# Optimization experiments

Hardware: AMD Instinct MI355X
Metric: run time of the kernel (lower is better)

## Reference

```python
import jax, jax.numpy as jnp
import numpy as np

NUM_HEADS = 12
HEAD_DIM = 64  # d_out // num_heads = 768 // 12


def setup_inputs() -> dict:
    key = jax.random.key(0)
    ks = jax.random.split(key, 6)
    b, s, d = 2, 2048, 768
    x = jax.random.normal(ks[0], (b, s, d), dtype=jnp.float32)
    sc = 1.0 / np.sqrt(d)
    Wq = jax.random.normal(ks[1], (d, d), dtype=jnp.float32) * sc
    Wk = jax.random.normal(ks[2], (d, d), dtype=jnp.float32) * sc
    Wv = jax.random.normal(ks[3], (d, d), dtype=jnp.float32) * sc
    Wo = jax.random.normal(ks[4], (d, d), dtype=jnp.float32) * sc
    bo = jnp.zeros((d,), dtype=jnp.float32)
    return {"x": x, "Wq": Wq, "Wk": Wk, "Wv": Wv, "Wo": Wo, "bo": bo}


def reference(x, Wq, Wk, Wv, Wo, bo):
    # Prefill from a fresh sliding-window KV cache: cache == new K/V,
    # standard causal (triu) mask. dropout=0 (eval).
    b, s, d = x.shape
    H, Dh = NUM_HEADS, HEAD_DIM

    def proj(W):  # torch Linear: x @ W^T, then split heads -> [b, H, s, Dh]
        return (x @ W.T).reshape(b, s, H, Dh).transpose(0, 2, 1, 3)

    q, k, v = proj(Wq), proj(Wk), proj(Wv)

    scores = jnp.einsum('bhqd,bhkd->bhqk', q, k)          # [b,H,s,s]
    causal = jnp.triu(jnp.ones((s, s), dtype=bool), k=1)  # future positions
    scores = jnp.where(causal[None, None], -jnp.inf, scores)
    attn = jax.nn.softmax(scores / np.sqrt(Dh), axis=-1)

    ctx = jnp.einsum('bhqk,bhkd->bhqd', attn, v)          # [b,H,s,Dh]
    ctx = ctx.transpose(0, 2, 1, 3).reshape(b, s, d)      # [b,s,d_out]
    return ctx @ Wo.T + bo
```

## Files before the change

### kernel.cpp

```cpp
#include <hip/hip_runtime.h>
#include <stdint.h>

typedef __attribute__((ext_vector_type(4))) float f32x4;
typedef __attribute__((ext_vector_type(8))) short s16x8;

#if __has_builtin(__builtin_amdgcn_exp2f)
#define EXP2(x) __builtin_amdgcn_exp2f(x)
#else
#define EXP2(x) exp2f(x)
#endif

#define GL2LDS(g, s)                                                        \
  __builtin_amdgcn_global_load_lds(                                         \
      (const __attribute__((address_space(1))) void*)(g),                   \
      (__attribute__((address_space(3))) void*)(s), 16, 0, 0)

__device__ __forceinline__ unsigned short tobf(float x) {
  uint32_t u = __builtin_bit_cast(uint32_t, x);
  u += 0x7fffu + ((u >> 16) & 1u);
  return (unsigned short)(u >> 16);
}

__device__ __forceinline__ uint32_t pk2(float lo, float hi) {
  return (uint32_t)tobf(lo) | ((uint32_t)tobf(hi) << 16);
}

__device__ __forceinline__ uint32_t pktrunc(float lo, float hi) {
  return __builtin_amdgcn_perm(__builtin_bit_cast(uint32_t, hi),
                               __builtin_bit_cast(uint32_t, lo), 0x07060302u);
}

__global__ __launch_bounds__(256) void cvt_all(
    const float* __restrict__ x,  const float* __restrict__ wq,
    const float* __restrict__ wk, const float* __restrict__ wv,
    const float* __restrict__ wo, unsigned short* __restrict__ outb) {
  int i = blockIdx.x * 256 + threadIdx.x;
  if (i >= 1376256) return;
  const float* in;
  int j;
  if (i < 786432) { in = x; j = i; }
  else {
    int k = i - 786432;
    int sel = k / 147456;
    j = k - sel * 147456;
    in = (sel == 0) ? wq : (sel == 1) ? wk : (sel == 2) ? wv : wo;
  }
  float4 v = reinterpret_cast<const float4*>(in)[j];
  uint2 o; o.x = pk2(v.x, v.y); o.y = pk2(v.z, v.w);
  reinterpret_cast<uint2*>(outb)[i] = o;
}

__global__ __launch_bounds__(128) void qkv_gemm(
    const unsigned short* __restrict__ xb,
    const unsigned short* __restrict__ wq,
    const unsigned short* __restrict__ wk,
    const unsigned short* __restrict__ wv,
    unsigned short* __restrict__ q_ws,
    unsigned short* __restrict__ k_ws,
    unsigned short* __restrict__ vt_ws) {
  __shared__ unsigned short As[2][2048];
  __shared__ unsigned short Bs[2][4096];
  const int t = threadIdx.x;
  const int l = t & 63, w = t >> 6;
  const int lr = l & 15, lg = l >> 4;

  const int id = (int)blockIdx.x;
  const int xcd = id & 7;
  const int g = id >> 3;
  const int nt = g % 18;
  const int tileM = ((g / 18) * 8 + xcd) * 64;
  const int wsel = nt / 6;
  const unsigned short* W = (wsel == 0) ? wq : ((wsel == 1) ? wk : wv);
  const int tileN = (nt % 6) * 128;

  const int srow = w * 16 + (l >> 2);
  const int scol = ((l & 3) ^ ((l >> 2) & 3)) * 8;

#define QSTAGE(buf, k0_)                                                       \
  do {                                                                         \
    GL2LDS(&xb[(tileM + srow) * 768 + (k0_) + scol],       &As[buf][w * 512]); \
    GL2LDS(&xb[(tileM + 32 + srow) * 768 + (k0_) + scol],  &As[buf][1024 + w * 512]); \
    _Pragma("unroll")                                                          \
    for (int i_ = 0; i_ < 4; ++i_)                                             \
      GL2LDS(&W[(tileN + i_ * 32 + srow) * 768 + (k0_) + scol],                \
             &Bs[buf][i_ * 1024 + w * 512]);                                   \
  } while (0)

  const int chf = ((lg ^ (lr & 3)) << 3);

  f32x4 acc[4][4];
  const f32x4 z4 = {0.f, 0.f, 0.f, 0.f};
#pragma unroll
  for (int i = 0; i < 4; ++i)
#pragma unroll
    for (int j = 0; j < 4; ++j) acc[i][j] = z4;

  QSTAGE(0, 0);
  __syncthreads();
  int c = 0;
  for (int it = 0; it < 24; ++it) {
    if (it < 23) QSTAGE(c ^ 1, (it + 1) * 32);
    s16x8 a[4], b[4];
#pragma unroll
    for (int mi = 0; mi < 4; ++mi)
      a[mi] = *(const s16x8*)&As[c][(mi * 16 + lr) * 32 + chf];
#pragma unroll
    for (int ni = 0; ni < 4; ++ni)
      b[ni] = *(const s16x8*)&Bs[c][(w * 64 + ni * 16 + lr) * 32 + chf];
    __builtin_amdgcn_s_setprio(1);
#pragma unroll
    for (int mi = 0; mi < 4; ++mi)
#pragma unroll
      for (int ni = 0; ni < 4; ++ni)
        acc[mi][ni] = __builtin_amdgcn_mfma_f32_16x16x32_bf16(a[mi], b[ni], acc[mi][ni], 0, 0, 0);
    __builtin_amdgcn_s_setprio(0);
    if (it < 23) {
      __syncthreads();
      c ^= 1;
    }
  }
#undef QSTAGE

#pragma unroll
  for (int mi = 0; mi < 4; ++mi)
#pragma unroll
    for (int ni = 0; ni < 4; ++ni) {
      int m0 = tileM + mi * 16 + lg * 4;
      int n = tileN + w * 64 + ni * 16 + lr;
      int bb = m0 >> 11, sq0 = m0 & 2047;
      int h = n >> 6, dh = n & 63;
      if (wsel == 0) {
#pragma unroll
        for (int r = 0; r < 4; ++r)
          q_ws[((bb * 12 + h) * 2048 + sq0 + r) * 64 + dh] =
              tobf(acc[mi][ni][r] * 0.18033688011112042f);
      } else if (wsel == 1) {
#pragma unroll
        for (int r = 0; r < 4; ++r)
          k_ws[((bb * 12 + h) * 2048 + sq0 + r) * 64 + dh] = tobf(acc[mi][ni][r]);
      } else {
        uint2 o;
        o.x = pk2(acc[mi][ni][0], acc[mi][ni][1]);
        o.y = pk2(acc[mi][ni][2], acc[mi][ni][3]);
        *(uint2*)&vt_ws[((bb * 12 + h) * 64 + dh) * 2048 + sq0] = o;
      }
    }
}

__global__ __launch_bounds__(128) void attn_kernel(
    const unsigned short* __restrict__ q_ws,
    const unsigned short* __restrict__ k_ws,
    const unsigned short* __restrict__ vt_ws,
    unsigned short* __restrict__ ctx) {
  __shared__ unsigned short Ks[2][4096];
  __shared__ unsigned short Vs[2][4096];

  const int t = threadIdx.x;
  const int l = t & 63, w = t >> 6;
  const int lr = l & 15, lg = l >> 4;

  const int id = (int)blockIdx.x;
  const int xcd = id & 7;
  const int g = id >> 3;
  const int qt = 63 - g / 3;
  const int bh = (g % 3) * 8 + xcd;

  const int rb = w * 8 + (l >> 3);
  const int gcol = ((l & 7) ^ (l >> 3)) * 8;
  const int krow = 8 * ((rb >> 2) & 3) + (rb & 3);
  const unsigned short* kgp  = &k_ws[(bh * 2048 + krow) * 64 + gcol];
  const unsigned short* vbase = &vt_ws[(bh * 64 + rb) * 2048 + gcol];

#define STAGE(buf, kt_)                                                \
  do {                                                                 \
    GL2LDS(kgp + (kt_) * 4096,           &Ks[buf][w * 512]);           \
    GL2LDS(kgp + (kt_) * 4096 + 2048,    &Ks[buf][1024 + w * 512]);    \
    GL2LDS(kgp + (kt_) * 4096 + 256,     &Ks[buf][2048 + w * 512]);    \
    GL2LDS(kgp + (kt_) * 4096 + 2304,    &Ks[buf][3072 + w * 512]);    \
    GL2LDS(vbase + (kt_) * 64,           &Vs[buf][w * 512]);           \
    GL2LDS(vbase + (kt_) * 64 + 32768,   &Vs[buf][1024 + w * 512]);    \
    GL2LDS(vbase + (kt_) * 64 + 65536,   &Vs[buf][2048 + w * 512]);    \
    GL2LDS(vbase + (kt_) * 64 + 98304,   &Vs[buf][3072 + w * 512]);    \
  } while (0)

  const int cks0 = (lg * 8) ^ ((lr & 7) << 3);
  const int cks1 = (32 + lg * 8) ^ ((lr & 7) << 3);

  const int bb = bh / 12, hh = bh % 12;
  const f32x4 z4 = {0.f, 0.f, 0.f, 0.f};

  const int ktmax = qt >> 1;
  const int qg = qt * 32 + w * 16 + lr;

  s16x8 qa[2];
#pragma unroll
  for (int kk = 0; kk < 2; ++kk)
    qa[kk] = *(const s16x8*)&q_ws[(bh * 2048 + qg) * 64 + kk * 32 + lg * 8];

  f32x4 o[4];
#pragma unroll
  for (int di = 0; di < 4; ++di) o[di] = z4;
  float lrun = 0.f;
  f32x4 s[4];

  STAGE(0, 0);
  __syncthreads();

  __builtin_amdgcn_s_setprio(1);
#pragma unroll
  for (int ni = 0; ni < 4; ++ni) {
    s16x8 kb0 = *(const s16x8*)&Ks[0][ni * 1024 + lr * 64 + cks0];
    s16x8 kb1 = *(const s16x8*)&Ks[0][ni * 1024 + lr * 64 + cks1];
    s[ni] = __builtin_amdgcn_mfma_f32_16x16x32_bf16(kb0, qa[0], z4, 0, 0, 0);
    s[ni] = __builtin_amdgcn_mfma_f32_16x16x32_bf16(kb1, qa[1], s[ni], 0, 0, 0);
  }
  __builtin_amdgcn_s_setprio(0);
  if (ktmax >= 1) STAGE(1, 1);

  int c = 0;
  for (int kt = 0; kt <= ktmax; ++kt) {
    if (kt == ktmax) {
#pragma unroll
      for (int ni = 0; ni < 4; ++ni)
#pragma unroll
        for (int r = 0; r < 4; ++r) {
          int kg_ = kt * 64 + ((ni & 1) << 5) + (lg << 3) + ((ni >> 1) << 2) + r;
          if (kg_ > qg) s[ni][r] = -1e30f;
        }
    }

#pragma unroll
    for (int ni = 0; ni < 4; ++ni)
#pragma unroll
      for (int r = 0; r < 4; ++r) s[ni][r] = EXP2(s[ni][r]);
    {
      float t0 = (s[0][0] + s[0][1]) + (s[0][2] + s[0][3]);
      float t1 = (s[1][0] + s[1][1]) + (s[1][2] + s[1][3]);
      float t2 = (s[2][0] + s[2][1]) + (s[2][2] + s[2][3]);
      float t3 = (s[3][0] + s[3][1]) + (s[3][2] + s[3][3]);
      lrun += (t0 + t1) + (t2 + t3);
    }

    s16x8 pa[2];
#pragma unroll
    for (int kk = 0; kk < 2; ++kk) {
      uint4 u;
      u.x = pktrunc(s[kk][0],     s[kk][1]);
      u.y = pktrunc(s[kk][2],     s[kk][3]);
      u.z = pktrunc(s[kk + 2][0], s[kk + 2][1]);
      u.w = pktrunc(s[kk + 2][2], s[kk + 2][3]);
      pa[kk] = __builtin_bit_cast(s16x8, u);
    }

    const bool have_next = (kt < ktmax);
    __builtin_amdgcn_s_setprio(1);
    if (have_next) {
      __syncthreads();
#pragma unroll
      for (int ni = 0; ni < 4; ++ni) {
        s16x8 kb0 = *(const s16x8*)&Ks[c ^ 1][ni * 1024 + lr * 64 + cks0];
        s16x8 kb1 = *(const s16x8*)&Ks[c ^ 1][ni * 1024 + lr * 64 + cks1];
        s[ni] = __builtin_amdgcn_mfma_f32_16x16x32_bf16(kb0, qa[0], z4, 0, 0, 0);
        s[ni] = __builtin_amdgcn_mfma_f32_16x16x32_bf16(kb1, qa[1], s[ni], 0, 0, 0);
      }
    }
#pragma unroll
    for (int di = 0; di < 4; ++di) {
      s16x8 vb0 = *(const s16x8*)&Vs[c][di * 1024 + lr * 64 + cks0];
      s16x8 vb1 = *(const s16x8*)&Vs[c][di * 1024 + lr * 64 + cks1];
      o[di] = __builtin_amdgcn_mfma_f32_16x16x32_bf16(vb0, pa[0], o[di], 0, 0, 0);
      o[di] = __builtin_amdgcn_mfma_f32_16x16x32_bf16(vb1, pa[1], o[di], 0, 0, 0);
    }
    __builtin_amdgcn_s_setprio(0);

    if (kt + 2 <= ktmax) {
      __syncthreads();
      STAGE(c, kt + 2);
    }
    c ^= 1;
  }

  float lt = lrun + __shfl_xor(lrun, 16);
  lt += __shfl_xor(lt, 32);
  const float rl = 1.0f / lt;
#pragma unroll
  for (int di = 0; di < 4; ++di) {
    uint2 ov;
    ov.x = pk2(o[di][0] * rl, o[di][1] * rl);
    ov.y = pk2(o[di][2] * rl, o[di][3] * rl);
    *(uint2*)&ctx[(bb * 2048 + qg) * 768 + hh * 64 + di * 16 + lg * 4] = ov;
  }
#undef STAGE
}

__global__ __launch_bounds__(64) void out_gemm(
    const unsigned short* __restrict__ ctxb,
    const unsigned short* __restrict__ wo,
    const float* __restrict__ bo,
    float* __restrict__ out) {
  __shared__ unsigned short As[2][2048];
  __shared__ unsigned short Bs[2][2048];
  const int l = threadIdx.x;
  const int lr = l & 15, lg = l >> 4;

  const int id = (int)blockIdx.x;
  const int xcd = id & 7;
  const int g = id >> 3;
  const int tileN = (g % 12) * 64;
  const int tileM = ((g / 12) * 8 + xcd) * 64;

  const int srow = l >> 2;
  const int scol = ((l & 3) ^ (srow & 3)) * 8;

#define OSTAGE(buf, k0_)                                                       \
  do {                                                                         \
    _Pragma("unroll")                                                          \
    for (int i_ = 0; i_ < 4; ++i_) {                                           \
      GL2LDS(&ctxb[(tileM + i_ * 16 + srow) * 768 + (k0_) + scol],             \
             &As[buf][i_ * 512]);                                              \
      GL2LDS(&wo  [(tileN + i_ * 16 + srow) * 768 + (k0_) + scol],             \
             &Bs[buf][i_ * 512]);                                              \
    }                                                                          \
  } while (0)

  const int chf = ((lg ^ (lr & 3)) << 3);

  f32x4 acc[4][4];
  const f32x4 z4 = {0.f, 0.f, 0.f, 0.f};
#pragma unroll
  for (int i = 0; i < 4; ++i)
#pragma unroll
    for (int j = 0; j < 4; ++j) acc[i][j] = z4;

  OSTAGE(0, 0);
  __syncthreads();
  int c = 0;
  for (int it = 0; it < 24; ++it) {
    if (it < 23) OSTAGE(c ^ 1, (it + 1) * 32);
    s16x8 a[4], b[4];
#pragma unroll
    for (int mi = 0; mi < 4; ++mi)
      a[mi] = *(const s16x8*)&As[c][(mi * 16 + lr) * 32 + chf];
#pragma unroll
    for (int ni = 0; ni < 4; ++ni)
      b[ni] = *(const s16x8*)&Bs[c][(ni * 16 + lr) * 32 + chf];
    __builtin_amdgcn_s_setprio(1);
#pragma unroll
    for (int mi = 0; mi < 4; ++mi)
#pragma unroll
      for (int ni = 0; ni < 4; ++ni)
        acc[mi][ni] = __builtin_amdgcn_mfma_f32_16x16x32_bf16(a[mi], b[ni], acc[mi][ni], 0, 0, 0);
    __builtin_amdgcn_s_setprio(0);
    if (it < 23) {
      __syncthreads();
      c ^= 1;
    }
  }
#undef OSTAGE

#pragma unroll
  for (int mi = 0; mi < 4; ++mi)
#pragma unroll
    for (int ni = 0; ni < 4; ++ni)
#pragma unroll
      for (int r = 0; r < 4; ++r) {
        int m = tileM + mi * 16 + lg * 4 + r;
        int n = tileN + ni * 16 + lr;
        out[m * 768 + n] = acc[mi][ni][r] + bo[n];
      }
}

extern "C" void kernel_launch(void* const* d_in, const int* in_sizes, int n_in,
                              void* d_out, int out_size, void* d_ws, size_t ws_size,
                              hipStream_t stream) {
  const float* x  = (const float*)d_in[0];
  const float* Wq = (const float*)d_in[1];
  const float* Wk = (const float*)d_in[2];
  const float* Wv = (const float*)d_in[3];
  const float* Wo = (const float*)d_in[4];
  const float* bo = (const float*)d_in[5];
  float* out = (float*)d_out;

  char* ws = (char*)d_ws;
  unsigned short* xb    = (unsigned short*)(ws);
  unsigned short* wqb   = (unsigned short*)(ws + 6291456);
  unsigned short* wkb   = (unsigned short*)(ws + 7471104);
  unsigned short* wvb   = (unsigned short*)(ws + 8650752);
  unsigned short* wob   = (unsigned short*)(ws + 9830400);
  unsigned short* q_ws  = (unsigned short*)(ws + 11010048);
  unsigned short* k_ws  = (unsigned short*)(ws + 17301504);
  unsigned short* vt_ws = (unsigned short*)(ws + 23592960);
  unsigned short* ctx   = (unsigned short*)(ws + 29884416);

  cvt_all<<<5376, 256, 0, stream>>>(x, Wq, Wk, Wv, Wo, (unsigned short*)ws);
  qkv_gemm<<<1152, 128, 0, stream>>>(xb, wqb, wkb, wvb, q_ws, k_ws, vt_ws);
  attn_kernel<<<1536, 128, 0, stream>>>(q_ws, k_ws, vt_ws, ctx);
  out_gemm<<<768, 64, 0, stream>>>(ctx, wob, bo, out);
}
```

Baseline: 88.96 us.

## Run QKV GEMM tile on a single wave and replace barriers with waitcnts

The QKV projection GEMM now uses one 64-lane wavefront per 64x128 tile instead of two waves. Each wave covers all 128 columns, with 32 accumulators instead of 16. Because only one wave touches the LDS buffers, the __syncthreads barriers are replaced by explicit s_waitcnt on vmcnt/lgkmcnt, which lets the next stage's global-to-LDS loads overlap compute. The cost is higher register pressure and fewer waves per block, which may reduce latency hiding.

```diff
diff --git a/kernel.cpp b/kernel.cpp
--- a/kernel.cpp
+++ b/kernel.cpp
@@ -50,7 +50,7 @@
   reinterpret_cast<uint2*>(outb)[i] = o;
 }
 
-__global__ __launch_bounds__(128) void qkv_gemm(
+__global__ __launch_bounds__(64) void qkv_gemm(
     const unsigned short* __restrict__ xb,
     const unsigned short* __restrict__ wq,
     const unsigned short* __restrict__ wk,
@@ -60,8 +60,7 @@
     unsigned short* __restrict__ vt_ws) {
   __shared__ unsigned short As[2][2048];
   __shared__ unsigned short Bs[2][4096];
-  const int t = threadIdx.x;
-  const int l = t & 63, w = t >> 6;
+  const int l = threadIdx.x;
   const int lr = l & 15, lg = l >> 4;
 
   const int id = (int)blockIdx.x;
@@ -73,60 +72,65 @@
   const unsigned short* W = (wsel == 0) ? wq : ((wsel == 1) ? wk : wv);
   const int tileN = (nt % 6) * 128;
 
-  const int srow = w * 16 + (l >> 2);
-  const int scol = ((l & 3) ^ ((l >> 2) & 3)) * 8;
+  const int srow = l >> 2;
+  const int scol = ((l & 3) ^ (srow & 3)) * 8;
 
 #define QSTAGE(buf, k0_)                                                       \
   do {                                                                         \
-    GL2LDS(&xb[(tileM + srow) * 768 + (k0_) + scol],       &As[buf][w * 512]); \
-    GL2LDS(&xb[(tileM + 32 + srow) * 768 + (k0_) + scol],  &As[buf][1024 + w * 512]); \
     _Pragma("unroll")                                                          \
     for (int i_ = 0; i_ < 4; ++i_)                                             \
-      GL2LDS(&W[(tileN + i_ * 32 + srow) * 768 + (k0_) + scol],                \
-             &Bs[buf][i_ * 1024 + w * 512]);                                   \
+      GL2LDS(&xb[(tileM + i_ * 16 + srow) * 768 + (k0_) + scol],               \
+             &As[buf][i_ * 512]);                                              \
+    _Pragma("unroll")                                                          \
+    for (int i_ = 0; i_ < 8; ++i_)                                             \
+      GL2LDS(&W[(tileN + i_ * 16 + srow) * 768 + (k0_) + scol],                \
+             &Bs[buf][i_ * 512]);                                              \
   } while (0)
 
   const int chf = ((lg ^ (lr & 3)) << 3);
 
-  f32x4 acc[4][4];
+  f32x4 acc[4][8];
   const f32x4 z4 = {0.f, 0.f, 0.f, 0.f};
 #pragma unroll
   for (int i = 0; i < 4; ++i)
 #pragma unroll
-    for (int j = 0; j < 4; ++j) acc[i][j] = z4;
+    for (int j = 0; j < 8; ++j) acc[i][j] = z4;
 
   QSTAGE(0, 0);
-  __syncthreads();
-  int c = 0;
   for (int it = 0; it < 24; ++it) {
-    if (it < 23) QSTAGE(c ^ 1, (it + 1) * 32);
-    s16x8 a[4], b[4];
+    const int c = it & 1;
+    if (it < 23) {
+      asm volatile("s_waitcnt lgkmcnt(0)" ::: "memory");
+      QSTAGE(c ^ 1, (it + 1) * 32);
+      asm volatile("s_waitcnt vmcnt(12)" ::: "memory");
+    } else {
+      asm volatile("s_waitcnt vmcnt(0)" ::: "memory");
+    }
+    __builtin_amdgcn_sched_barrier(0);
+
+    s16x8 a[4], b[8];
 #pragma unroll
     for (int mi = 0; mi < 4; ++mi)
       a[mi] = *(const s16x8*)&As[c][(mi * 16 + lr) * 32 + chf];
 #pragma unroll
-    for (int ni = 0; ni < 4; ++ni)
-      b[ni] = *(const s16x8*)&Bs[c][(w * 64 + ni * 16 + lr) * 32 + chf];
+    for (int ni = 0; ni < 8; ++ni)
+      b[ni] = *(const s16x8*)&Bs[c][(ni * 16 + lr) * 32 + chf];
     __builtin_amdgcn_s_setprio(1);
 #pragma unroll
     for (int mi = 0; mi < 4; ++mi)
 #pragma unroll
-      for (int ni = 0; ni < 4; ++ni)
+      for (int ni = 0; ni < 8; ++ni)
         acc[mi][ni] = __builtin_amdgcn_mfma_f32_16x16x32_bf16(a[mi], b[ni], acc[mi][ni], 0, 0, 0);
     __builtin_amdgcn_s_setprio(0);
-    if (it < 23) {
-      __syncthreads();
-      c ^= 1;
-    }
   }
 #undef QSTAGE
 
 #pragma unroll
   for (int mi = 0; mi < 4; ++mi)
 #pragma unroll
-    for (int ni = 0; ni < 4; ++ni) {
+    for (int ni = 0; ni < 8; ++ni) {
       int m0 = tileM + mi * 16 + lg * 4;
-      int n = tileN + w * 64 + ni * 16 + lr;
+      int n = tileN + ni * 16 + lr;
       int bb = m0 >> 11, sq0 = m0 & 2047;
       int h = n >> 6, dh = n & 63;
       if (wsel == 0) {
@@ -393,7 +397,7 @@
   unsigned short* ctx   = (unsigned short*)(ws + 29884416);
 
   cvt_all<<<5376, 256, 0, stream>>>(x, Wq, Wk, Wv, Wo, (unsigned short*)ws);
-  qkv_gemm<<<1152, 128, 0, stream>>>(xb, wqb, wkb, wvb, q_ws, k_ws, vt_ws);
+  qkv_gemm<<<1152, 64, 0, stream>>>(xb, wqb, wkb, wvb, q_ws, k_ws, vt_ws);
   attn_kernel<<<1536, 128, 0, stream>>>(q_ws, k_ws, vt_ws, ctx);
   out_gemm<<<768, 64, 0, stream>>>(ctx, wob, bo, out);
 }
```

After: 89.90 us. No clear change (+1.1%).
